# Kernel tuning notes

Measured on AMD Instinct MI355X. Metric: run time of the kernel, lower is better.

The kernel has to match this reference:

```python
import jax, jax.numpy as jnp
import numpy as np

B, T, C, H = 4, 2048, 1024, 16
HD = C // H  # head dim = 64

def setup_inputs() -> dict:
    key = jax.random.key(0)
    k1, k2, k3 = jax.random.split(key, 3)
    x = jax.random.normal(k1, (B, T, C), dtype=jnp.float32)
    w_attn = jax.random.normal(k2, (C, 3 * C), dtype=jnp.float32) * 0.02
    w_proj = jax.random.normal(k3, (C, C), dtype=jnp.float32) * 0.02
    return {"x": x, "w_attn": w_attn, "w_proj": w_proj}

def reference(x, w_attn, w_proj):
    b, t, c = x.shape
    qkv = x @ w_attn  # [B,T,3C]
    q, k, v = jnp.split(qkv, 3, axis=-1)
    # [B,T,C] -> [B,H,T,HD]
    def heads(z):
        return z.reshape(b, t, H, HD).transpose(0, 2, 1, 3)
    q, k, v = heads(q), heads(k), heads(v)
    scale = 1.0 / jnp.sqrt(jnp.float32(HD))
    att = jnp.einsum('bhqd,bhkd->bhqk', q, k) * scale  # [B,H,T,T]
    causal = jnp.tril(jnp.ones((t, t), dtype=bool))
    att = jnp.where(causal[None, None], att, -jnp.inf)
    att = jax.nn.softmax(att, axis=-1)
    y = jnp.einsum('bhqk,bhkd->bhqd', att, v)  # [B,H,T,HD]
    y = y.transpose(0, 2, 1, 3).reshape(b, t, c)
    return y @ w_proj
```

## Files before the change

### kernel.cpp

```cpp
#include <hip/hip_runtime.h>
#include <hip/hip_bf16.h>

typedef short bf16x8 __attribute__((ext_vector_type(8)));
typedef short short4v __attribute__((ext_vector_type(4)));
typedef float f32x4 __attribute__((ext_vector_type(4)));
typedef float f32x16 __attribute__((ext_vector_type(16)));

template <bool V> struct BoolC { static constexpr bool value = V; };

__device__ __forceinline__ short f2b(float f) {
  __hip_bfloat16 h = __float2bfloat16(f);
  union { __hip_bfloat16 h; short s; } u; u.h = h; return u.s;
}

__device__ __forceinline__ unsigned cvtpk_bf16(float lo, float hi) {
  unsigned r;
  asm("v_cvt_pk_bf16_f32 %0, %1, %2" : "=v"(r) : "v"(lo), "v"(hi));
  return r;
}

__device__ __forceinline__ f32x16 mfma32(bf16x8 a, bf16x8 b, f32x16 c) {
  return __builtin_amdgcn_mfma_f32_32x32x16_bf16(a, b, c, 0, 0, 0);
}

template <int N> __device__ __forceinline__ void vmwait() {
  if constexpr (N == 0) asm volatile("s_waitcnt vmcnt(0)" ::: "memory");
  else if constexpr (N == 1) asm volatile("s_waitcnt vmcnt(1)" ::: "memory");
  else if constexpr (N == 2) asm volatile("s_waitcnt vmcnt(2)" ::: "memory");
  else if constexpr (N == 3) asm volatile("s_waitcnt vmcnt(3)" ::: "memory");
  else if constexpr (N == 4) asm volatile("s_waitcnt vmcnt(4)" ::: "memory");
  else if constexpr (N == 5) asm volatile("s_waitcnt vmcnt(5)" ::: "memory");
  else if constexpr (N == 6) asm volatile("s_waitcnt vmcnt(6)" ::: "memory");
  else if constexpr (N == 7) asm volatile("s_waitcnt vmcnt(7)" ::: "memory");
  else asm volatile("s_waitcnt vmcnt(8)" ::: "memory");
}

__device__ __forceinline__ void async_copy16(const short* g, short* l) {
  __builtin_amdgcn_global_load_lds((const __attribute__((address_space(1))) void*)g,
                                   (__attribute__((address_space(3))) void*)l, 16, 0, 0);
}

__global__ __launch_bounds__(256) void pre_kernel(const float* __restrict__ x, short* __restrict__ xb,
                                                  const float* __restrict__ wa, short* __restrict__ waT,
                                                  const float* __restrict__ wp, short* __restrict__ wpT,
                                                  float qscale) {
  const int tid = threadIdx.x;
  const int blk = blockIdx.x;
  if (blk < 8192) {
    const int i = blk * 256 + tid;
    const float4 v = ((const float4*)x)[i];
    short4v o;
    o[0] = f2b(v.x); o[1] = f2b(v.y); o[2] = f2b(v.z); o[3] = f2b(v.w);
    ((short4v*)xb)[i] = o;
    return;
  }
  __shared__ float t[32][33];
  const float* in; short* out;
  int idx, gxb, Cn, qrows; float qs;
  if (blk < 11264) { idx = blk - 8192;  in = wa; out = waT; gxb = 96; Cn = 3072; qrows = 1024; qs = qscale; }
  else             { idx = blk - 11264; in = wp; out = wpT; gxb = 32; Cn = 1024; qrows = 0;    qs = 1.0f; }
  const int bx = idx % gxb, by = idx / gxb;
  const int tx = tid & 31, ty = tid >> 5;
  const int c0 = bx * 32, r0 = by * 32;
#pragma unroll
  for (int yy = 0; yy < 32; yy += 8)
    t[ty + yy][tx] = in[(size_t)(r0 + ty + yy) * Cn + (c0 + tx)];
  __syncthreads();
#pragma unroll
  for (int yy = 0; yy < 32; yy += 8) {
    const int orow = c0 + ty + yy;
    float v = t[tx][ty + yy];
    if (orow < qrows) v *= qs;
    out[(size_t)orow * 1024 + (r0 + tx)] = f2b(v);
  }
}

template <int BN, typename OutT, bool VFUSE>
__global__ __launch_bounds__(256, 2) void gemm2b_kernel(const short* __restrict__ A,
                                                        const short* __restrict__ Bt,
                                                        OutT* __restrict__ C,
                                                        short* __restrict__ vTo,
                                                        int M, int N, int K) {
  constexpr int NB = BN / 64;
  constexpr int NBU = BN / 32;
  constexpr int NSTREAM = NBU + 4;
  __shared__ short ldsA[2][128 * 64];
  __shared__ short ldsB[2][BN * 64];

  const int tid = threadIdx.x;
  const int w = tid >> 6, lane = tid & 63;
  const int quad = lane >> 4, l16 = lane & 15;
  const int wn = w * (BN / 4);

  const int gx = gridDim.x;
  const int nwg = gx * gridDim.y;
  const int flat = blockIdx.y * gx + blockIdx.x;
  const int swz = (flat & 7) * (nwg >> 3) + (flat >> 3);
  const int bn = swz % gx, bm = swz / gx;
  const int m0 = bm * 128, n0 = bn * BN;

  const int rsub = lane >> 3;
  const int cl = (lane & 7) ^ rsub;
  const short* pAsrc = A + (size_t)(m0 + w * 8 + rsub) * K + cl * 8;
  const short* pBsrc = Bt + (size_t)(n0 + w * 8 + rsub) * K + cl * 8;

  f32x4 acc[8][NB] = {};
  bf16x8 bfr[NB][2];

  auto issue = [&](int i, int buf, int tt) {
    if (i < NBU)
      async_copy16(pBsrc + (size_t)(i * 32) * K + tt * 64, &ldsB[buf][(i * 32 + w * 8) * 64]);
    else
      async_copy16(pAsrc + (size_t)((i - NBU) * 32) * K + tt * 64,
                   &ldsA[buf][((i - NBU) * 32 + w * 8) * 64]);
  };
  auto readA = [&](bf16x8 (&af)[2][2], int buf, int P) {
#pragma unroll
    for (int mm = 0; mm < 2; ++mm)
#pragma unroll
      for (int kh = 0; kh < 2; ++kh)
        af[mm][kh] = *(const bf16x8*)&ldsA[buf][(P * 32 + mm * 16 + l16) * 64 +
                                                (((kh * 4 + quad) ^ (l16 & 7)) * 8)];
  };
  auto readB = [&](int buf) {
#pragma unroll
    for (int nf = 0; nf < NB; ++nf)
#pragma unroll
      for (int kh = 0; kh < 2; ++kh)
        bfr[nf][kh] = *(const bf16x8*)&ldsB[buf][(wn + nf * 16 + l16) * 64 +
                                                 (((kh * 4 + quad) ^ (l16 & 7)) * 8)];
  };

#define PHASE(P)                                                                               \
  {                                                                                            \
    constexpr int ISS0 = (NSTREAM + 3) >> 2, ISS1 = (NSTREAM + 2) >> 2,                        \
                  ISS2 = (NSTREAM + 1) >> 2;                                                   \
    constexpr int CUM = ((P) > 0 ? ISS0 : 0) + ((P) > 1 ? ISS1 : 0) + ((P) > 2 ? ISS2 : 0);    \
    constexpr int GS = NSTREAM - (NBU + 1 + (P)) + CUM;                                        \
    constexpr int GL = 3 - (P);                                                                \
    if constexpr ((P) == 0) asm volatile("s_waitcnt lgkmcnt(0)" ::: "memory");                 \
    if constexpr (LAST) vmwait<GL>(); else vmwait<GS>();                                       \
    __builtin_amdgcn_s_barrier();                                                              \
    bf16x8 af[2][2];                                                                           \
    readA(af, buf, (P));                                                                       \
    if constexpr ((P) == 0) readB(buf);                                                        \
    if constexpr (!LAST) {                                                                     \
      constexpr int NI = (NSTREAM + 3 - (P)) >> 2;                                             \
      _Pragma("unroll") for (int ii = 0; ii < NI; ++ii) issue(CUM + ii, buf ^ 1, t + 1);       \
    }                                                                                          \
    __builtin_amdgcn_s_setprio(1);                                                             \
    _Pragma("unroll") for (int mm = 0; mm < 2; ++mm)                                           \
    _Pragma("unroll") for (int nf = 0; nf < NB; ++nf) {                                        \
      acc[(P)*2 + mm][nf] = __builtin_amdgcn_mfma_f32_16x16x32_bf16(af[mm][0], bfr[nf][0],     \
                                                                    acc[(P)*2 + mm][nf], 0, 0, 0); \
      acc[(P)*2 + mm][nf] = __builtin_amdgcn_mfma_f32_16x16x32_bf16(af[mm][1], bfr[nf][1],     \
                                                                    acc[(P)*2 + mm][nf], 0, 0, 0); \
    }                                                                                          \
    __builtin_amdgcn_s_setprio(0);                                                             \
  }

#pragma unroll
  for (int i = 0; i < NSTREAM; ++i) issue(i, 0, 0);

  const int NT = K >> 6;
  auto tile = [&](int t, int buf, auto lastc) {
    constexpr bool LAST = decltype(lastc)::value;
    PHASE(0)
    PHASE(1)
    PHASE(2)
    PHASE(3)
  };
  for (int t = 0; t < NT - 1; ++t) tile(t, t & 1, BoolC<false>{});
  tile(NT - 1, (NT - 1) & 1, BoolC<true>{});
#undef PHASE

  (void)M;
#pragma unroll
  for (int mf = 0; mf < 8; ++mf)
#pragma unroll
    for (int nf = 0; nf < NB; ++nf) {
      const int col = n0 + wn + nf * 16 + l16;
      const int row0 = m0 + mf * 16 + quad * 4;
      if constexpr (VFUSE) {
        if (col < 2048) {
#pragma unroll
          for (int r = 0; r < 4; ++r)
            C[(size_t)(row0 + r) * 2048 + col] = f2b(acc[mf][nf][r]);
        } else {
          const int dp = col - 2048;
          const int bh64 = ((row0 >> 11) * 16 + (dp >> 6)) * 64 + (dp & 63);
          const int t0 = row0 & 2047;
          short4v v4;
#pragma unroll
          for (int r = 0; r < 4; ++r) v4[r] = f2b(acc[mf][nf][r]);
          *(short4v*)&vTo[(size_t)bh64 * 2048 + t0] = v4;
        }
      } else {
#pragma unroll
        for (int r = 0; r < 4; ++r) {
          const int row = row0 + r;
          if constexpr (sizeof(OutT) == 4)
            C[(size_t)row * N + col] = acc[mf][nf][r];
          else
            C[(size_t)row * N + col] = f2b(acc[mf][nf][r]);
        }
      }
    }
}

__global__ __launch_bounds__(256, 2) void attn_kernel(const short* __restrict__ qk,
                                                      const short* __restrict__ vT,
                                                      short* __restrict__ y) {
  constexpr int T = 2048, C2 = 2048, Cc = 1024, HD = 64;
  const int f = blockIdx.y * 8 + blockIdx.x;
  const int bh = (f & 7) * 8 + ((f >> 3) & 7);
  const int xb = f >> 6;
  const int b = bh >> 4, h = bh & 15;
  const int tid = threadIdx.x, lane = tid & 63, wave = tid >> 6;
  const int l32 = lane & 31, hi = lane >> 5;

  __shared__ short Ksb[2][64 * 64];
  __shared__ short Vtb[2][64 * 64];

  const size_t base = (size_t)b * T * C2;
  const int qcol = h * HD, kcol = 1024 + h * HD;
  const size_t vtbase = (size_t)bh * HD * T;

  const int r8 = lane >> 3;
  const int cg8 = ((lane & 7) ^ r8) * 8;
  const short* gk[2];
  const short* gv[2];
  short* lk[2][2]; short* lv[2][2];
#pragma unroll
  for (int t8 = 0; t8 < 2; t8++) {
    const int row = wave * 16 + t8 * 8 + r8;
    gk[t8] = qk + base + (size_t)row * C2 + kcol + cg8;
    gv[t8] = vT + vtbase + (size_t)row * T + cg8;
#pragma unroll
    for (int bu = 0; bu < 2; bu++) {
      lk[bu][t8] = &Ksb[bu][(wave * 16 + t8 * 8) * 64];
      lv[bu][t8] = &Vtb[bu][(wave * 16 + t8 * 8) * 64];
    }
  }
  const int rs7 = l32 & 7;

  bf16x8 ones;
#pragma unroll
  for (int i = 0; i < 8; i++) ones[i] = (short)0x3F80;

  for (int half = 0; half < 2; half++) {
    const int t = half ? xb : (15 - xb);
    const int q0 = t * 128;
    const int jmax = 2 * t + 1;
    const int jd = 2 * t + (wave >> 1);
    const int qrow = q0 + wave * 32 + l32;

    bf16x8 qf[4];
    {
      const short* qp = qk + base + (size_t)qrow * C2 + qcol + hi * 8;
#pragma unroll
      for (int wk = 0; wk < 4; wk++) qf[wk] = *(const bf16x8*)(qp + wk * 16);
    }

    f32x16 o0 = {}, o1 = {}, lC = {};

    async_copy16(gk[0], lk[0][0]);
    async_copy16(gk[1], lk[0][1]);
    async_copy16(gv[0], lv[0][0]);
    async_copy16(gv[1], lv[0][1]);

    for (int j = 0; j <= jmax; j++) {
      const int cur = j & 1;
      __syncthreads();

      if (j < jmax) {
        const size_t ko = (size_t)(j + 1) * 64 * C2;
        const int vo = (j + 1) * 64;
        async_copy16(gk[0] + ko, lk[cur ^ 1][0]);
        async_copy16(gk[1] + ko, lk[cur ^ 1][1]);
        async_copy16(gv[0] + vo, lv[cur ^ 1][0]);
        async_copy16(gv[1] + vo, lv[cur ^ 1][1]);
      }

      if (j > jd) continue;

      const bool up = (64 * j + 32) <= (q0 + wave * 32 + 31);

      f32x16 st0 = {}, st1 = {};
      __builtin_amdgcn_s_setprio(1);
#pragma unroll
      for (int wk = 0; wk < 4; wk++) {
        const bf16x8 k0 = *(const bf16x8*)&Ksb[cur][l32 * 64 + (((2 * wk + hi) ^ rs7) * 8)];
        st0 = mfma32(k0, qf[wk], st0);
      }
      if (up) {
#pragma unroll
        for (int wk = 0; wk < 4; wk++) {
          const bf16x8 k1 = *(const bf16x8*)&Ksb[cur][(32 + l32) * 64 + (((2 * wk + hi) ^ rs7) * 8)];
          st1 = mfma32(k1, qf[wk], st1);
        }
      }
      __builtin_amdgcn_s_setprio(0);

      if (j == jd) {
#pragma unroll
        for (int r = 0; r < 16; r++) {
          const int kvl = 64 * j + (r & 3) + 8 * (r >> 2) + 4 * hi;
          if (kvl > qrow) st0[r] = -INFINITY;
          if (up && (kvl + 32 > qrow)) st1[r] = -INFINITY;
        }
      }

      bf16x8 vf00, vf01, vf10, vf11, vf02, vf03, vf12, vf13;
      vf00 = *(const bf16x8*)&Vtb[cur][l32 * 64 + (((0 + hi) ^ rs7) * 8)];
      vf01 = *(const bf16x8*)&Vtb[cur][l32 * 64 + (((2 + hi) ^ rs7) * 8)];
      vf10 = *(const bf16x8*)&Vtb[cur][(32 + l32) * 64 + (((0 + hi) ^ rs7) * 8)];
      vf11 = *(const bf16x8*)&Vtb[cur][(32 + l32) * 64 + (((2 + hi) ^ rs7) * 8)];
      if (up) {
        vf02 = *(const bf16x8*)&Vtb[cur][l32 * 64 + (((4 + hi) ^ rs7) * 8)];
        vf03 = *(const bf16x8*)&Vtb[cur][l32 * 64 + (((6 + hi) ^ rs7) * 8)];
        vf12 = *(const bf16x8*)&Vtb[cur][(32 + l32) * 64 + (((4 + hi) ^ rs7) * 8)];
        vf13 = *(const bf16x8*)&Vtb[cur][(32 + l32) * 64 + (((6 + hi) ^ rs7) * 8)];
      }

#pragma unroll
      for (int r = 0; r < 16; r++) st0[r] = __builtin_amdgcn_exp2f(st0[r]);
      bf16x8 pa0, pa1, pa2, pa3;
      {
        unsigned a0 = cvtpk_bf16(st0[0], st0[1]), c0 = cvtpk_bf16(st0[2], st0[3]);
        unsigned b0 = cvtpk_bf16(st0[4], st0[5]), d0 = cvtpk_bf16(st0[6], st0[7]);
        asm volatile("v_permlane32_swap_b32 %0, %1" : "+v"(a0), "+v"(b0));
        asm volatile("v_permlane32_swap_b32 %0, %1" : "+v"(c0), "+v"(d0));
        union { unsigned u[4]; bf16x8 v; } p; p.u[0] = a0; p.u[1] = c0; p.u[2] = b0; p.u[3] = d0;
        pa0 = p.v;
        unsigned a1 = cvtpk_bf16(st0[8], st0[9]), c1 = cvtpk_bf16(st0[10], st0[11]);
        unsigned b1 = cvtpk_bf16(st0[12], st0[13]), d1 = cvtpk_bf16(st0[14], st0[15]);
        asm volatile("v_permlane32_swap_b32 %0, %1" : "+v"(a1), "+v"(b1));
        asm volatile("v_permlane32_swap_b32 %0, %1" : "+v"(c1), "+v"(d1));
        union { unsigned u[4]; bf16x8 v; } q; q.u[0] = a1; q.u[1] = c1; q.u[2] = b1; q.u[3] = d1;
        pa1 = q.v;
      }
      if (up) {
#pragma unroll
        for (int r = 0; r < 16; r++) st1[r] = __builtin_amdgcn_exp2f(st1[r]);
        unsigned a2 = cvtpk_bf16(st1[0], st1[1]), c2 = cvtpk_bf16(st1[2], st1[3]);
        unsigned b2 = cvtpk_bf16(st1[4], st1[5]), d2 = cvtpk_bf16(st1[6], st1[7]);
        asm volatile("v_permlane32_swap_b32 %0, %1" : "+v"(a2), "+v"(b2));
        asm volatile("v_permlane32_swap_b32 %0, %1" : "+v"(c2), "+v"(d2));
        union { unsigned u[4]; bf16x8 v; } p; p.u[0] = a2; p.u[1] = c2; p.u[2] = b2; p.u[3] = d2;
        pa2 = p.v;
        unsigned a3 = cvtpk_bf16(st1[8], st1[9]), c3 = cvtpk_bf16(st1[10], st1[11]);
        unsigned b3 = cvtpk_bf16(st1[12], st1[13]), d3 = cvtpk_bf16(st1[14], st1[15]);
        asm volatile("v_permlane32_swap_b32 %0, %1" : "+v"(a3), "+v"(b3));
        asm volatile("v_permlane32_swap_b32 %0, %1" : "+v"(c3), "+v"(d3));
        union { unsigned u[4]; bf16x8 v; } q; q.u[0] = a3; q.u[1] = c3; q.u[2] = b3; q.u[3] = d3;
        pa3 = q.v;
      }

      __builtin_amdgcn_s_setprio(1);
      lC = mfma32(pa0, ones, lC);
      lC = mfma32(pa1, ones, lC);
      o0 = mfma32(pa0, vf00, o0);
      o0 = mfma32(pa1, vf01, o0);
      o1 = mfma32(pa0, vf10, o1);
      o1 = mfma32(pa1, vf11, o1);
      if (up) {
        lC = mfma32(pa2, ones, lC);
        lC = mfma32(pa3, ones, lC);
        o0 = mfma32(pa2, vf02, o0);
        o0 = mfma32(pa3, vf03, o0);
        o1 = mfma32(pa2, vf12, o1);
        o1 = mfma32(pa3, vf13, o1);
      }
      __builtin_amdgcn_s_setprio(0);
    }

#pragma unroll
    for (int r = 0; r < 16; r++) {
      const int rq = (r & 3) + 8 * (r >> 2) + 4 * hi;
      const int row_g = q0 + wave * 32 + rq;
      const float inv = 1.0f / lC[r];
      short* yp = y + (size_t)(b * T + row_g) * Cc + h * HD;
      yp[l32] = f2b(o0[r] * inv);
      yp[32 + l32] = f2b(o1[r] * inv);
    }
  }
}

extern "C" void kernel_launch(void* const* d_in, const int* in_sizes, int n_in,
                              void* d_out, int out_size, void* d_ws, size_t ws_size,
                              hipStream_t stream) {
  constexpr int B = 4, T = 2048, C = 1024;
  constexpr int M = B * T;
  constexpr int N1 = 3 * C;
  const float* x      = (const float*)d_in[0];
  const float* w_attn = (const float*)d_in[1];
  const float* w_proj = (const float*)d_in[2];
  float* out = (float*)d_out;

  char* ws = (char*)d_ws;
  short* xb   = (short*)(ws + 0);
  short* waT  = (short*)(ws + 16777216);
  short* wpT  = (short*)(ws + 23068672);
  short* qkb  = (short*)(ws + 25165824);
  short* vT   = (short*)(ws + 58720256);
  short* yb   = (short*)(ws + 75497472);

  const float qscale = 0.125f * 1.44269504088896340736f;

  pre_kernel<<<12288, 256, 0, stream>>>(x, xb, w_attn, waT, w_proj, wpT, qscale);
  gemm2b_kernel<192, short, true><<<dim3(N1 / 192, M / 128), 256, 0, stream>>>(
      xb, waT, qkb, vT, M, N1, C);
  attn_kernel<<<dim3(8, B * 16), 256, 0, stream>>>(qkb, vT, yb);
  gemm2b_kernel<128, float, false><<<dim3(C / 128, M / 128), 256, 0, stream>>>(
      yb, wpT, out, nullptr, M, C, C);
}
```

Before: 218.6 us.

## Rewrite GEMM kernel with 512-thread blocks, K=32 tiles and simpler double buffering

```diff
diff --git a/kernel.cpp b/kernel.cpp
--- a/kernel.cpp
+++ b/kernel.cpp
@@ -21,18 +21,6 @@
 
 __device__ __forceinline__ f32x16 mfma32(bf16x8 a, bf16x8 b, f32x16 c) {
   return __builtin_amdgcn_mfma_f32_32x32x16_bf16(a, b, c, 0, 0, 0);
-}
-
-template <int N> __device__ __forceinline__ void vmwait() {
-  if constexpr (N == 0) asm volatile("s_waitcnt vmcnt(0)" ::: "memory");
-  else if constexpr (N == 1) asm volatile("s_waitcnt vmcnt(1)" ::: "memory");
-  else if constexpr (N == 2) asm volatile("s_waitcnt vmcnt(2)" ::: "memory");
-  else if constexpr (N == 3) asm volatile("s_waitcnt vmcnt(3)" ::: "memory");
-  else if constexpr (N == 4) asm volatile("s_waitcnt vmcnt(4)" ::: "memory");
-  else if constexpr (N == 5) asm volatile("s_waitcnt vmcnt(5)" ::: "memory");
-  else if constexpr (N == 6) asm volatile("s_waitcnt vmcnt(6)" ::: "memory");
-  else if constexpr (N == 7) asm volatile("s_waitcnt vmcnt(7)" ::: "memory");
-  else asm volatile("s_waitcnt vmcnt(8)" ::: "memory");
 }
 
 __device__ __forceinline__ void async_copy16(const short* g, short* l) {
@@ -76,21 +64,22 @@
 }
 
 template <int BN, typename OutT, bool VFUSE>
-__global__ __launch_bounds__(256, 2) void gemm2b_kernel(const short* __restrict__ A,
-                                                        const short* __restrict__ Bt,
-                                                        OutT* __restrict__ C,
-                                                        short* __restrict__ vTo,
-                                                        int M, int N, int K) {
+__global__ __launch_bounds__(512, 4) void gemm_hi_kernel(const short* __restrict__ A,
+                                                         const short* __restrict__ Bt,
+                                                         OutT* __restrict__ C,
+                                                         short* __restrict__ vTo,
+                                                         int M, int N, int K) {
   constexpr int NB = BN / 64;
-  constexpr int NBU = BN / 32;
-  constexpr int NSTREAM = NBU + 4;
-  __shared__ short ldsA[2][128 * 64];
-  __shared__ short ldsB[2][BN * 64];
+  constexpr int NBU = BN / 16;
+  constexpr int U = NBU + 8;
+  constexpr int BSHORT = (8 + NBU) * 512;
+  __shared__ short lds[2][BSHORT];
 
   const int tid = threadIdx.x;
   const int w = tid >> 6, lane = tid & 63;
   const int quad = lane >> 4, l16 = lane & 15;
-  const int wn = w * (BN / 4);
+  const int mh = w >> 2;
+  const int wn = (w & 3) * (BN / 4);
 
   const int gx = gridDim.x;
   const int nwg = gx * gridDim.y;
@@ -99,88 +88,63 @@
   const int bn = swz % gx, bm = swz / gx;
   const int m0 = bm * 128, n0 = bn * BN;
 
-  const int rsub = lane >> 3;
-  const int cl = (lane & 7) ^ rsub;
-  const short* pAsrc = A + (size_t)(m0 + w * 8 + rsub) * K + cl * 8;
-  const short* pBsrc = Bt + (size_t)(n0 + w * 8 + rsub) * K + cl * 8;
-
-  f32x4 acc[8][NB] = {};
-  bf16x8 bfr[NB][2];
-
-  auto issue = [&](int i, int buf, int tt) {
-    if (i < NBU)
-      async_copy16(pBsrc + (size_t)(i * 32) * K + tt * 64, &ldsB[buf][(i * 32 + w * 8) * 64]);
-    else
-      async_copy16(pAsrc + (size_t)((i - NBU) * 32) * K + tt * 64,
-                   &ldsA[buf][((i - NBU) * 32 + w * 8) * 64]);
+  const int r16 = lane >> 2, pc = lane & 3;
+  const int cl = pc ^ ((r16 ^ (r16 >> 2)) & 3);
+  const int us = (w * U) >> 3, ue = ((w + 1) * U) >> 3;
+  const int nu = ue - us;
+  const short* gsrc[3];
+  int loff[3];
+#pragma unroll
+  for (int i = 0; i < 3; ++i) {
+    const int u = us + i;
+    if (i < nu) {
+      if (u < NBU) { gsrc[i] = Bt + (size_t)(n0 + u * 16 + r16) * K + cl * 8; loff[i] = 4096 + u * 512; }
+      else { const int a = u - NBU; gsrc[i] = A + (size_t)(m0 + a * 16 + r16) * K + cl * 8; loff[i] = a * 512; }
+    } else { gsrc[i] = Bt; loff[i] = 0; }
+  }
+
+  f32x4 acc[4][NB] = {};
+  const int s16 = (l16 ^ (l16 >> 2)) & 3;
+
+  auto stage = [&](int buf, int t) {
+#pragma unroll
+    for (int i = 0; i < 3; ++i)
+      if (i < nu) async_copy16(gsrc[i] + t * 32, &lds[buf][loff[i]]);
   };
-  auto readA = [&](bf16x8 (&af)[2][2], int buf, int P) {
-#pragma unroll
-    for (int mm = 0; mm < 2; ++mm)
-#pragma unroll
-      for (int kh = 0; kh < 2; ++kh)
-        af[mm][kh] = *(const bf16x8*)&ldsA[buf][(P * 32 + mm * 16 + l16) * 64 +
-                                                (((kh * 4 + quad) ^ (l16 & 7)) * 8)];
-  };
-  auto readB = [&](int buf) {
+
+  stage(0, 0);
+
+  const int NT = K >> 5;
+  for (int t = 0; t < NT; ++t) {
+    const int buf = t & 1;
+    asm volatile("s_waitcnt lgkmcnt(0)" ::: "memory");
+    asm volatile("s_waitcnt vmcnt(0)" ::: "memory");
+    __builtin_amdgcn_s_barrier();
+    asm volatile("" ::: "memory");
+    if (t + 1 < NT) stage(buf ^ 1, t + 1);
+    bf16x8 af[4], bf[NB];
+#pragma unroll
+    for (int mf = 0; mf < 4; ++mf)
+      af[mf] = *(const bf16x8*)&lds[buf][(mh * 64 + mf * 16 + l16) * 32 + ((quad ^ s16) * 8)];
 #pragma unroll
     for (int nf = 0; nf < NB; ++nf)
-#pragma unroll
-      for (int kh = 0; kh < 2; ++kh)
-        bfr[nf][kh] = *(const bf16x8*)&ldsB[buf][(wn + nf * 16 + l16) * 64 +
-                                                 (((kh * 4 + quad) ^ (l16 & 7)) * 8)];
-  };
-
-#define PHASE(P)                                                                               \
-  {                                                                                            \
-    constexpr int ISS0 = (NSTREAM + 3) >> 2, ISS1 = (NSTREAM + 2) >> 2,                        \
-                  ISS2 = (NSTREAM + 1) >> 2;                                                   \
-    constexpr int CUM = ((P) > 0 ? ISS0 : 0) + ((P) > 1 ? ISS1 : 0) + ((P) > 2 ? ISS2 : 0);    \
-    constexpr int GS = NSTREAM - (NBU + 1 + (P)) + CUM;                                        \
-    constexpr int GL = 3 - (P);                                                                \
-    if constexpr ((P) == 0) asm volatile("s_waitcnt lgkmcnt(0)" ::: "memory");                 \
-    if constexpr (LAST) vmwait<GL>(); else vmwait<GS>();                                       \
-    __builtin_amdgcn_s_barrier();                                                              \
-    bf16x8 af[2][2];                                                                           \
-    readA(af, buf, (P));                                                                       \
-    if constexpr ((P) == 0) readB(buf);                                                        \
-    if constexpr (!LAST) {                                                                     \
-      constexpr int NI = (NSTREAM + 3 - (P)) >> 2;                                             \
-      _Pragma("unroll") for (int ii = 0; ii < NI; ++ii) issue(CUM + ii, buf ^ 1, t + 1);       \
-    }                                                                                          \
-    __builtin_amdgcn_s_setprio(1);                                                             \
-    _Pragma("unroll") for (int mm = 0; mm < 2; ++mm)                                           \
-    _Pragma("unroll") for (int nf = 0; nf < NB; ++nf) {                                        \
-      acc[(P)*2 + mm][nf] = __builtin_amdgcn_mfma_f32_16x16x32_bf16(af[mm][0], bfr[nf][0],     \
-                                                                    acc[(P)*2 + mm][nf], 0, 0, 0); \
-      acc[(P)*2 + mm][nf] = __builtin_amdgcn_mfma_f32_16x16x32_bf16(af[mm][1], bfr[nf][1],     \
-                                                                    acc[(P)*2 + mm][nf], 0, 0, 0); \
-    }                                                                                          \
-    __builtin_amdgcn_s_setprio(0);                                                             \
-  }
-
-#pragma unroll
-  for (int i = 0; i < NSTREAM; ++i) issue(i, 0, 0);
-
-  const int NT = K >> 6;
-  auto tile = [&](int t, int buf, auto lastc) {
-    constexpr bool LAST = decltype(lastc)::value;
-    PHASE(0)
-    PHASE(1)
-    PHASE(2)
-    PHASE(3)
-  };
-  for (int t = 0; t < NT - 1; ++t) tile(t, t & 1, BoolC<false>{});
-  tile(NT - 1, (NT - 1) & 1, BoolC<true>{});
-#undef PHASE
+      bf[nf] = *(const bf16x8*)&lds[buf][4096 + (wn + nf * 16 + l16) * 32 + ((quad ^ s16) * 8)];
+    __builtin_amdgcn_s_setprio(1);
+#pragma unroll
+    for (int mf = 0; mf < 4; ++mf)
+#pragma unroll
+      for (int nf = 0; nf < NB; ++nf)
+        acc[mf][nf] = __builtin_amdgcn_mfma_f32_16x16x32_bf16(af[mf], bf[nf], acc[mf][nf], 0, 0, 0);
+    __builtin_amdgcn_s_setprio(0);
+  }
 
   (void)M;
 #pragma unroll
-  for (int mf = 0; mf < 8; ++mf)
+  for (int mf = 0; mf < 4; ++mf)
 #pragma unroll
     for (int nf = 0; nf < NB; ++nf) {
       const int col = n0 + wn + nf * 16 + l16;
-      const int row0 = m0 + mf * 16 + quad * 4;
+      const int row0 = m0 + mh * 64 + mf * 16 + quad * 4;
       if constexpr (VFUSE) {
         if (col < 2048) {
 #pragma unroll
@@ -409,9 +373,9 @@
   const float qscale = 0.125f * 1.44269504088896340736f;
 
   pre_kernel<<<12288, 256, 0, stream>>>(x, xb, w_attn, waT, w_proj, wpT, qscale);
-  gemm2b_kernel<192, short, true><<<dim3(N1 / 192, M / 128), 256, 0, stream>>>(
+  gemm_hi_kernel<192, short, true><<<dim3(N1 / 192, M / 128), 512, 0, stream>>>(
       xb, waT, qkb, vT, M, N1, C);
   attn_kernel<<<dim3(8, B * 16), 256, 0, stream>>>(qkb, vT, yb);
-  gemm2b_kernel<128, float, false><<<dim3(C / 128, M / 128), 256, 0, stream>>>(
+  gemm_hi_kernel<128, float, false><<<dim3(C / 128, M / 128), 512, 0, stream>>>(
       yb, wpT, out, nullptr, M, C, C);
 }
```

Measured after the change: 230.2 us. 5.3% more time.
